# Kernel optimization log

Measured on AMD Instinct MI355X. Metric: run time of the kernel, lower is better.

The kernel has to match this reference:

```python
import jax, jax.numpy as jnp
import numpy as np

# Dimensions
B, T, H = 4, 4096, 2048          # batch, seq, hidden
NH = 16                           # total hash heads = (max_ngram-1)*n_head_per_ngram
PER_HEAD_VOCAB = 100000
DH = 64                           # per-head embedding dim
E = NH * DH                       # engram_hidden_size = 1024
G = 4                             # hc_mult
K = 4                             # kernel_size
DIL = 3                           # dilation = max_ngram_size
EPS_RMS = 1.1920929e-07           # torch RMSNorm default eps (fp32 finfo eps)
EPS_SC = 1e-5                     # ShortConv RMSNorm eps


def setup_inputs() -> dict:
    key = jax.random.key(0)
    ks = jax.random.split(key, 12)
    hidden_states = jax.random.normal(ks[0], (T, B, H), dtype=jnp.float32)
    hash_ids = jax.random.randint(ks[1], (B, T, NH), 0, PER_HEAD_VOCAB)
    emb_table = jax.random.normal(ks[2], (NH * PER_HEAD_VOCAB, DH), dtype=jnp.float32)
    s = 0.02
    key_W = jax.random.normal(ks[3], (G, H, E), dtype=jnp.float32) * s
    key_b = jax.random.normal(ks[4], (G, H), dtype=jnp.float32) * s
    value_W = jax.random.normal(ks[5], (H, E), dtype=jnp.float32) * s
    value_b = jax.random.normal(ks[6], (H,), dtype=jnp.float32) * s
    norm1_w = jnp.ones((G, H), dtype=jnp.float32)
    norm2_w = jnp.ones((G, H), dtype=jnp.float32)
    sc_norm_w = jnp.ones((G, H), dtype=jnp.float32)
    conv_w = jax.random.normal(ks[7], (G * H, K), dtype=jnp.float32) * 0.1
    return {"hidden_states": hidden_states, "hash_ids": hash_ids, "emb_table": emb_table,
            "key_W": key_W, "key_b": key_b, "value_W": value_W, "value_b": value_b,
            "norm1_w": norm1_w, "norm2_w": norm2_w, "sc_norm_w": sc_norm_w, "conv_w": conv_w}


def _rms(x, eps):
    return x * jax.lax.rsqrt(jnp.mean(x * x, axis=-1, keepdims=True) + eps)


def reference(hidden_states, hash_ids, emb_table, key_W, key_b, value_W, value_b,
              norm1_w, norm2_w, sc_norm_w, conv_w):
    # --- precompute_embeddings: hashed multi-head gather ---
    offsets = jnp.arange(NH, dtype=hash_ids.dtype) * PER_HEAD_VOCAB
    emb = emb_table[hash_ids + offsets]              # [B,T,NH,DH]
    emb = emb.reshape(B, T, E)                       # [B,T,E]

    # --- forward ---
    hs = jnp.transpose(hidden_states, (1, 0, 2))     # [B,T,H]
    # per-group key projection + RMSNorm (vectorized over G)
    keys = jnp.einsum('bte,ghe->btgh', emb, key_W) + key_b   # [B,T,G,H]
    nk = _rms(keys, EPS_RMS) * norm1_w               # [B,T,G,H]
    nq = _rms(hs, EPS_RMS)[:, :, None, :] * norm2_w  # [B,T,G,H]
    gate = jnp.sum(nk * nq, axis=-1) / np.sqrt(H)    # [B,T,G]
    gate = jnp.sqrt(jnp.maximum(jnp.abs(gate), 1e-6)) * jnp.sign(gate)
    gate = jax.nn.sigmoid(gate)[..., None]           # [B,T,G,1]
    value = gate * (emb @ value_W.T + value_b)[:, :, None, :]   # [B,T,G,H]

    # --- ShortConv: per-group RMSNorm -> causal dilated depthwise conv -> SiLU ---
    xn = _rms(value, EPS_SC) * sc_norm_w             # [B,T,G,H]
    x_bct = xn.reshape(B, T, G * H).transpose(0, 2, 1)  # [B,G*H,T]
    y = jax.lax.conv_general_dilated(
        x_bct, conv_w[:, None, :],                   # rhs [C,1,K]
        window_strides=(1,), padding=[((K - 1) * DIL, 0)],
        rhs_dilation=(DIL,), dimension_numbers=('NCH', 'OIH', 'NCH'),
        feature_group_count=G * H)                   # [B,G*H,T]
    y = jax.nn.silu(y)
    y = y.transpose(0, 2, 1).reshape(B, T, G, H)

    out = (value + y).mean(axis=2)                   # [B,T,H]
    return jnp.transpose(out, (1, 0, 2))             # [S,B,H]
```

## Files before the change

### kernel.cpp

```cpp
#include <hip/hip_runtime.h>
#include <hip/hip_bf16.h>

#define BB 4
#define TT 4096
#define HH 2048
#define NHH 16
#define VOC 100000
#define EE 1024
#define GG 4
#define BT (BB*TT)
#define NKEY (GG*HH)
#define NTOT (NKEY+HH)
#define NPART 32
#define TCV 48

static constexpr float EPS_RMS = 1.1920929e-07f;
static constexpr float EPS_SC  = 1e-5f;
static constexpr float INV_SQRT_H = 0.02209708691207961f;

using f32x4 = __attribute__((ext_vector_type(4))) float;
using s8v   = __attribute__((ext_vector_type(8))) short;
using gvoid = __attribute__((address_space(1))) const void;
using lvoid = __attribute__((address_space(3))) void;

__device__ __forceinline__ unsigned short f2bf(float f){
  union { __hip_bfloat16 h; unsigned short u; } cv;
  cv.h = __float2bfloat16(f);
  return cv.u;
}
__device__ __forceinline__ float bf2f(unsigned short u){
  union { float f; unsigned u; } cv;
  cv.u = ((unsigned)u) << 16;
  return cv.f;
}

__global__ __launch_bounds__(256) void convw_kern(const float* __restrict__ kW,
    const float* __restrict__ vW, unsigned short* __restrict__ Wc){
  const long idx  = (long)blockIdx.x*256 + threadIdx.x;
  const long base = idx*4;
  const long KN   = (long)NKEY*EE;
  float4 v;
  if (base < KN) v = *(const float4*)(kW + base);
  else           v = *(const float4*)(vW + (base - KN));
  ushort4 o; o.x=f2bf(v.x); o.y=f2bf(v.y); o.z=f2bf(v.z); o.w=f2bf(v.w);
  *(ushort4*)(Wc + base) = o;
}

__global__ __launch_bounds__(256) void prep_kern(const int* __restrict__ hids,
    const float* __restrict__ table, unsigned short* __restrict__ emb,
    const float* __restrict__ hs, float* __restrict__ rq,
    unsigned short* __restrict__ hsbf){
  const int p = blockIdx.x, tid = threadIdx.x;
  const int e = tid*4, head = e>>6, d = e&63;
  const long row = (long)hids[p*NHH + head] + (long)head*VOC;
  const float4 v = *(const float4*)(table + row*64 + d);
  ushort4 o; o.x=f2bf(v.x); o.y=f2bf(v.y); o.z=f2bf(v.z); o.w=f2bf(v.w);
  *(ushort4*)(emb + (size_t)p*EE + e) = o;
  const int b = p>>12, t = p&4095;
  const float* hrow = hs + ((size_t)t*BB + b)*HH;
  const int e8 = tid*8;
  float4 v0 = *(const float4*)(hrow+e8);
  float4 v1 = *(const float4*)(hrow+e8+4);
  ushort4 hb0; hb0.x=f2bf(v0.x); hb0.y=f2bf(v0.y); hb0.z=f2bf(v0.z); hb0.w=f2bf(v0.w);
  ushort4 hb1; hb1.x=f2bf(v1.x); hb1.y=f2bf(v1.y); hb1.z=f2bf(v1.z); hb1.w=f2bf(v1.w);
  *(ushort4*)(hsbf + (size_t)p*HH + e8)     = hb0;
  *(ushort4*)(hsbf + (size_t)p*HH + e8 + 4) = hb1;
  float s = v0.x*v0.x+v0.y*v0.y+v0.z*v0.z+v0.w*v0.w
          + v1.x*v1.x+v1.y*v1.y+v1.z*v1.z+v1.w*v1.w;
  #pragma unroll
  for (int of=32;of>=1;of>>=1) s += __shfl_xor(s,of);
  __shared__ float red[4];
  if ((tid&63)==0) red[tid>>6] = s;
  __syncthreads();
  if (tid==0){
    float tot = red[0]+red[1]+red[2]+red[3];
    rq[p] = rsqrtf(tot*(1.0f/HH) + EPS_RMS);
  }
}

__global__ __launch_bounds__(512, 2) void gemm8(
    const unsigned short* __restrict__ A, const unsigned short* __restrict__ Bw,
    const float* __restrict__ key_b, const float* __restrict__ value_b,
    const float* __restrict__ n1w, const float* __restrict__ n2w,
    const unsigned short* __restrict__ hsbf, unsigned short* __restrict__ vlinb,
    float* __restrict__ sumsqp, float* __restrict__ dotp, float* __restrict__ vsqp)
{
  __shared__ unsigned short sh[65536];
  const int tid = threadIdx.x, w = tid>>6, l = tid&63;
  const int wm = w>>2, wn = w&3;
  const int lg = l&15, lr = l>>4;
  const int tN = blockIdx.x, tM = blockIdx.y;
  const int Mrow0 = tM*256, Nrow0 = tN*256;

  const int lp = l>>3, lcs = (l&7)^lp;
  const size_t aoffT = (size_t)(Mrow0 + w*16 + lp)*EE + lcs*8;
  const size_t boffT = (size_t)(Nrow0 + w*16 + lp)*EE + lcs*8;
  const int c0 = lr ^ (lg&7);
  const unsigned aBase = (unsigned)(wm*8192 + lg*64);
  const unsigned bBase = (unsigned)(16384 + (wn>>1)*8192 + (wn&1)*4096 + lg*64);

  f32x4 acc[8][4] = {};
  s8v aR[2][4], bR[2][4];

#define STAGEH(ISB, H, KT, SB) { \
    const unsigned short* s0_ = ((ISB) ? (Bw + boffT) : (A + aoffT)) + (H)*131072 + (KT)*64; \
    const unsigned d0_ = (SB)*32768 + (ISB)*16384 + (H)*8192 + w*1024; \
    __builtin_amdgcn_global_load_lds((gvoid*)s0_,        (lvoid*)(sh + d0_),       16, 0, 0); \
    __builtin_amdgcn_global_load_lds((gvoid*)(s0_+8192), (lvoid*)(sh + d0_ + 512), 16, 0, 0); \
  }

#define BAR() { asm volatile("" ::: "memory"); __builtin_amdgcn_s_barrier(); asm volatile("" ::: "memory"); }

#define RD_A(CB, KK, MH) { \
    const unsigned short* p_ = sh + (CB)*32768 + aBase; \
    const unsigned ck_ = (unsigned)((c0 ^ ((KK)<<2))<<3); \
    aR[KK][0] = *(const s8v*)(p_ + ((MH)*4+0)*1024 + ck_); \
    aR[KK][1] = *(const s8v*)(p_ + ((MH)*4+1)*1024 + ck_); \
    aR[KK][2] = *(const s8v*)(p_ + ((MH)*4+2)*1024 + ck_); \
    aR[KK][3] = *(const s8v*)(p_ + ((MH)*4+3)*1024 + ck_); }

#define RD_B(CB, KK) { \
    const unsigned short* p_ = sh + (CB)*32768 + bBase; \
    const unsigned ck_ = (unsigned)((c0 ^ ((KK)<<2))<<3); \
    bR[KK][0] = *(const s8v*)(p_ + 0*1024 + ck_); \
    bR[KK][1] = *(const s8v*)(p_ + 1*1024 + ck_); \
    bR[KK][2] = *(const s8v*)(p_ + 2*1024 + ck_); \
    bR[KK][3] = *(const s8v*)(p_ + 3*1024 + ck_); }

#define MM(MH, KK) { \
    __builtin_amdgcn_s_setprio(1); \
    _Pragma("unroll") \
    for (int mf=0; mf<4; mf++) \
      _Pragma("unroll") \
      for (int nf=0; nf<4; nf++) \
        acc[(MH)*4+mf][nf] = __builtin_amdgcn_mfma_f32_16x16x32_bf16(aR[KK][mf], bR[KK][nf], acc[(MH)*4+mf][nf], 0,0,0); \
    __builtin_amdgcn_s_setprio(0); }

#define PH0(CB, SB, STKT, DOST) { \
    asm volatile("s_waitcnt vmcnt(0)" ::: "memory"); \
    BAR(); \
    if (DOST) { STAGEH(0, 0, STKT, SB); STAGEH(0, 1, STKT, SB); } \
    RD_A(CB, 0, 0); RD_B(CB, 0); \
    asm volatile("s_waitcnt lgkmcnt(0)" ::: "memory"); \
    __builtin_amdgcn_sched_barrier(0); \
    MM(0, 0); \
    BAR(); }

#define PH1(CB, SB, STKT, DOST) { \
    RD_A(CB, 1, 0); RD_B(CB, 1); \
    if (DOST) { STAGEH(1, 0, STKT, SB); STAGEH(1, 1, STKT, SB); } \
    BAR(); \
    asm volatile("s_waitcnt lgkmcnt(0)" ::: "memory"); \
    __builtin_amdgcn_sched_barrier(0); \
    MM(0, 1); \
    BAR(); }

#define PH2(CB) { \
    RD_A(CB, 0, 1); \
    BAR(); \
    asm volatile("s_waitcnt lgkmcnt(0)" ::: "memory"); \
    __builtin_amdgcn_sched_barrier(0); \
    MM(1, 0); \
    BAR(); }

#define PH3(CB) { \
    RD_A(CB, 1, 1); \
    BAR(); \
    asm volatile("s_waitcnt lgkmcnt(0)" ::: "memory"); \
    __builtin_amdgcn_sched_barrier(0); \
    MM(1, 1); \
    BAR(); }

  STAGEH(0,0,0,0); STAGEH(0,1,0,0); STAGEH(1,0,0,0); STAGEH(1,1,0,0);

  #pragma unroll 1
  for (int i=0; i<8; i++){
    const int kt = 2*i;
    PH0(0, 1, kt+1, true);
    PH1(0, 1, kt+1, true);
    PH2(0);
    PH3(0);
    PH0(1, 0, kt+2, (kt+2)<16);
    PH1(1, 0, kt+2, (kt+2)<16);
    PH2(1);
    PH3(1);
  }

#undef STAGEH
#undef BAR
#undef RD_A
#undef RD_B
#undef MM
#undef PH0
#undef PH1
#undef PH2
#undef PH3

  const bool isK = (Nrow0 < NKEY);
  float bias[4], cw[4];
  #pragma unroll
  for (int nf=0; nf<4; nf++){
    const int n = Nrow0 + wn*64 + nf*16 + lg;
    if (isK){ bias[nf] = key_b[n]; cw[nf] = n1w[n]*n2w[n]; }
    else    { bias[nf] = value_b[n-NKEY]; cw[nf] = 0.f; }
  }

  if (isK){
    unsigned short* hsT = sh;
    const int colbase = Nrow0 & (HH-1);
    #pragma unroll
    for (int pass=0; pass<16; pass++){
      const int r = pass*16 + (tid>>5);
      const int c8 = (tid&31)*8;
      const int p = Mrow0 + r;
      s8v wv = *(const s8v*)(hsbf + (size_t)p*HH + colbase + c8);
      *(s8v*)(hsT + r*256 + (c8 ^ (((r>>2)&3)<<4))) = wv;
    }
    __syncthreads();
    const int g = Nrow0 >> 11;
    const int slot = (tN&7)*4 + wn;
    #pragma unroll
    for (int mfa=0; mfa<8; mfa++){
      #pragma unroll
      for (int rr=0; rr<4; rr++){
        const int rowl = wm*128 + mfa*16 + lr*4 + rr;
        const int p = Mrow0 + rowl;
        float ssq=0.f, dt=0.f;
        #pragma unroll
        for (int nf=0; nf<4; nf++){
          const float c = acc[mfa][nf][rr] + bias[nf];
          const float hv = bf2f(hsT[rowl*256 + wn*64 + (((nf^lr))<<4) + lg]);
          ssq += c*c;
          dt  += c * cw[nf] * hv;
        }
        #pragma unroll
        for (int o=1;o<16;o<<=1){ ssq += __shfl_xor(ssq,o); dt += __shfl_xor(dt,o); }
        if (lg==0){
          sumsqp[(size_t)(p*GG+g)*NPART + slot] = ssq;
          dotp  [(size_t)(p*GG+g)*NPART + slot] = dt;
        }
      }
    }
  } else {
    const int slot = (tN-32)*4 + wn;
    const int h0 = Nrow0 - NKEY + wn*64;
    const int pbase = Mrow0 + wm*128;
    #pragma unroll
    for (int mfa=0; mfa<8; mfa++){
      #pragma unroll
      for (int rr=0; rr<4; rr++){
        const int p = pbase + mfa*16 + lr*4 + rr;
        float ssq=0.f;
        #pragma unroll
        for (int nf=0; nf<4; nf++){
          const float c = acc[mfa][nf][rr] + bias[nf];
          vlinb[(size_t)p*HH + h0 + nf*16 + lg] = f2bf(c);
          ssq += c*c;
        }
        #pragma unroll
        for (int o=1;o<16;o<<=1){ ssq += __shfl_xor(ssq,o); }
        if (lg==0) vsqp[(size_t)p*NPART + slot] = ssq;
      }
    }
  }
}

__global__ __launch_bounds__(256) void scal_kern(const float* __restrict__ sumsqp,
    const float* __restrict__ dotp, const float* __restrict__ vsqp,
    const float* __restrict__ rq, float* __restrict__ gate, float* __restrict__ av){
  const int i = blockIdx.x*256 + threadIdx.x;
  const int p = i>>2;
  float ss=0.f, dd=0.f, vv=0.f;
  #pragma unroll
  for (int j=0;j<NPART;j++){ ss += sumsqp[(size_t)i*NPART+j]; dd += dotp[(size_t)i*NPART+j]; }
  #pragma unroll
  for (int j=0;j<NPART;j++){ vv += vsqp[(size_t)p*NPART+j]; }
  const float rk = rsqrtf(ss*(1.0f/HH) + EPS_RMS);
  const float gv = rk * rq[p] * dd * INV_SQRT_H;
  const float sgn = (gv>0.f)?1.f:((gv<0.f)?-1.f:0.f);
  const float g1 = sqrtf(fmaxf(fabsf(gv),1e-6f))*sgn;
  const float gt = 1.f/(1.f+__expf(-g1));
  const float msvl = vv*(1.0f/HH);
  const float a = gt * rsqrtf(gt*gt*msvl + EPS_SC);
  gate[i]=gt; av[i]=a;
}

__device__ __forceinline__ ushort4 ldrow(const unsigned short* __restrict__ v, int b, int t, int h0){
  if (t < 0){ ushort4 z; z.x=0;z.y=0;z.z=0;z.w=0; return z; }
  return *(const ushort4*)(v + (size_t)((b<<12)|t)*HH + h0);
}
__device__ __forceinline__ void ldav(const float* __restrict__ av, int b, int t, float* a){
  if (t < 0){ a[0]=0.f;a[1]=0.f;a[2]=0.f;a[3]=0.f; }
  else { const float4 x = *(const float4*)(av + (size_t)((b<<12)|t)*GG);
         a[0]=x.x;a[1]=x.y;a[2]=x.z;a[3]=x.w; }
}

__global__ __launch_bounds__(256) void conv2_kern(const unsigned short* __restrict__ vlinb,
    const float* __restrict__ gate, const float* __restrict__ av,
    const float* __restrict__ conv_w, const float* __restrict__ scw,
    float* __restrict__ out){
  const int bx = blockIdx.x;
  const int b  = blockIdx.y;
  const int t0 = (bx>>1)*TCV;
  const int h0 = (bx&1)*1024 + threadIdx.x*4;

  float cwv[4][4][4];
  float sc4[4][4];
  #pragma unroll
  for (int g=0; g<4; g++){
    #pragma unroll
    for (int j2=0; j2<4; j2++){
      const int c = g*HH + h0 + j2;
      const float4 wv = *(const float4*)(conv_w + (size_t)c*4);
      cwv[g][j2][0]=wv.x; cwv[g][j2][1]=wv.y; cwv[g][j2][2]=wv.z; cwv[g][j2][3]=wv.w;
      sc4[g][j2] = scw[c];
    }
  }

  #pragma unroll 1
  for (int r=0; r<3; r++){
    const int tf = t0 + r;
    ushort4 w0 = ldrow(vlinb, b, tf-9, h0);
    ushort4 w1 = ldrow(vlinb, b, tf-6, h0);
    ushort4 w2 = ldrow(vlinb, b, tf-3, h0);
    ushort4 w3; w3.x=0;w3.y=0;w3.z=0;w3.w=0;
    #pragma unroll
    for (int j=0; j<16; j++){
      const int t = tf + 3*j;
      if (t < TT){
        const int p = (b<<12)|t;
        w3 = *(const ushort4*)(vlinb + (size_t)p*HH + h0);
        float a0[4],a1[4],a2[4],a3[4];
        ldav(av, b, t-9, a0); ldav(av, b, t-6, a1); ldav(av, b, t-3, a2); ldav(av, b, t, a3);
        float gt4[4];
        { const float4 x = *(const float4*)(gate + (size_t)p*GG);
          gt4[0]=x.x; gt4[1]=x.y; gt4[2]=x.z; gt4[3]=x.w; }
        float v0[4],v1[4],v2[4],v3[4];
        v0[0]=bf2f(w0.x); v0[1]=bf2f(w0.y); v0[2]=bf2f(w0.z); v0[3]=bf2f(w0.w);
        v1[0]=bf2f(w1.x); v1[1]=bf2f(w1.y); v1[2]=bf2f(w1.z); v1[3]=bf2f(w1.w);
        v2[0]=bf2f(w2.x); v2[1]=bf2f(w2.y); v2[2]=bf2f(w2.z); v2[3]=bf2f(w2.w);
        v3[0]=bf2f(w3.x); v3[1]=bf2f(w3.y); v3[2]=bf2f(w3.z); v3[3]=bf2f(w3.w);
        float4 ov;
        float res[4];
        #pragma unroll
        for (int j2=0; j2<4; j2++){
          float acc = 0.f;
          #pragma unroll
          for (int g=0; g<4; g++){
            float y = cwv[g][j2][0]*a0[g]*v0[j2]
                    + cwv[g][j2][1]*a1[g]*v1[j2]
                    + cwv[g][j2][2]*a2[g]*v2[j2]
                    + cwv[g][j2][3]*a3[g]*v3[j2];
            y *= sc4[g][j2];
            const float sy = y * (1.f/(1.f+__expf(-y)));
            acc += gt4[g]*v3[j2] + sy;
          }
          res[j2] = acc*0.25f;
        }
        ov.x=res[0]; ov.y=res[1]; ov.z=res[2]; ov.w=res[3];
        *(float4*)(out + ((size_t)t*BB + b)*HH + h0) = ov;
      }
      w0=w1; w1=w2; w2=w3;
    }
  }
}

extern "C" void kernel_launch(void* const* d_in, const int* in_sizes, int n_in,
                              void* d_out, int out_size, void* d_ws, size_t ws_size,
                              hipStream_t stream){
  (void)in_sizes; (void)n_in; (void)out_size; (void)ws_size;
  const float* hs    = (const float*)d_in[0];
  const int*   hids  = (const int*)d_in[1];
  const float* table = (const float*)d_in[2];
  const float* keyW  = (const float*)d_in[3];
  const float* keyB  = (const float*)d_in[4];
  const float* valW  = (const float*)d_in[5];
  const float* valB  = (const float*)d_in[6];
  const float* n1w   = (const float*)d_in[7];
  const float* n2w   = (const float*)d_in[8];
  const float* scw   = (const float*)d_in[9];
  const float* convw = (const float*)d_in[10];
  float* out = (float*)d_out;

  char* ws = (char*)d_ws;
  size_t off = 0;
  unsigned short* emb   = (unsigned short*)(ws+off); off += (size_t)BT*EE*2;
  unsigned short* Wc    = (unsigned short*)(ws+off); off += (size_t)NTOT*EE*2;
  unsigned short* vlinb = (unsigned short*)(ws+off); off += (size_t)BT*HH*2;
  unsigned short* hsbf  = (unsigned short*)(ws+off); off += (size_t)BT*HH*2;
  float* sumsqp = (float*)(ws+off); off += (size_t)BT*GG*NPART*4;
  float* dotp   = (float*)(ws+off); off += (size_t)BT*GG*NPART*4;
  float* vsqp   = (float*)(ws+off); off += (size_t)BT*NPART*4;
  float* rq     = (float*)(ws+off); off += (size_t)BT*4;
  float* gate   = (float*)(ws+off); off += (size_t)BT*GG*4;
  float* av     = (float*)(ws+off); off += (size_t)BT*GG*4;

  convw_kern<<<(NTOT*EE/4)/256, 256, 0, stream>>>(keyW, valW, Wc);
  prep_kern<<<BT, 256, 0, stream>>>(hids, table, emb, hs, rq, hsbf);
  dim3 gg(NTOT/256, BT/256);
  gemm8<<<gg, 512, 0, stream>>>(emb, Wc, keyB, valB, n1w, n2w, hsbf, vlinb, sumsqp, dotp, vsqp);
  scal_kern<<<(BT*GG)/256, 256, 0, stream>>>(sumsqp, dotp, vsqp, rq, gate, av);
  dim3 cg(((TT + TCV - 1)/TCV)*2, BB);
  conv2_kern<<<cg, 256, 0, stream>>>(vlinb, gate, av, convw, scw, out);
}
```

Before: 569.6 us.

## Restructure GEMM main loop with register double-buffering, XCD swizzle, and packed partials

The GEMM main loop is reorganized so LDS fragment reads for the next k-step and the next tile are issued while MFMAs run, removing most per-phase barriers and lgkmcnt waits. Workgroup IDs are remapped with an 8-way swizzle so tiles sharing A/B rows land on the same XCD for L2 reuse. The key epilogue now reads hidden-state values directly from global memory and reduces partial sums through LDS, writing sumsq and dot as a packed float2. The separate sumsq and dot buffers are merged, so the scalar kernel does one vector load per partial. This risks higher register pressure from the double-buffered fragments, plus scattered global loads in the epilogue.

```diff
diff --git a/kernel.cpp b/kernel.cpp
--- a/kernel.cpp
+++ b/kernel.cpp
@@ -19,6 +19,7 @@
 static constexpr float INV_SQRT_H = 0.02209708691207961f;
 
 using f32x4 = __attribute__((ext_vector_type(4))) float;
+using f32x2 = __attribute__((ext_vector_type(2))) float;
 using s8v   = __attribute__((ext_vector_type(8))) short;
 using gvoid = __attribute__((address_space(1))) const void;
 using lvoid = __attribute__((address_space(3))) void;
@@ -83,13 +84,15 @@
     const float* __restrict__ key_b, const float* __restrict__ value_b,
     const float* __restrict__ n1w, const float* __restrict__ n2w,
     const unsigned short* __restrict__ hsbf, unsigned short* __restrict__ vlinb,
-    float* __restrict__ sumsqp, float* __restrict__ dotp, float* __restrict__ vsqp)
+    f32x2* __restrict__ sdp, float* __restrict__ vsqp)
 {
   __shared__ unsigned short sh[65536];
   const int tid = threadIdx.x, w = tid>>6, l = tid&63;
   const int wm = w>>2, wn = w&3;
   const int lg = l&15, lr = l>>4;
-  const int tN = blockIdx.x, tM = blockIdx.y;
+  const int wg  = blockIdx.x;
+  const int swz = (wg&7)*320 + (wg>>3);
+  const int tM  = swz/40, tN = swz - tM*40;
   const int Mrow0 = tM*256, Nrow0 = tN*256;
 
   const int lp = l>>3, lcs = (l&7)^lp;
@@ -100,7 +103,7 @@
   const unsigned bBase = (unsigned)(16384 + (wn>>1)*8192 + (wn&1)*4096 + lg*64);
 
   f32x4 acc[8][4] = {};
-  s8v aR[2][4], bR[2][4];
+  s8v aR0[4], aR1[4], bR0[4], bR1[4];
 
 #define STAGEH(ISB, H, KT, SB) { \
     const unsigned short* s0_ = ((ISB) ? (Bw + boffT) : (A + aoffT)) + (H)*131072 + (KT)*64; \
@@ -108,138 +111,127 @@
     __builtin_amdgcn_global_load_lds((gvoid*)s0_,        (lvoid*)(sh + d0_),       16, 0, 0); \
     __builtin_amdgcn_global_load_lds((gvoid*)(s0_+8192), (lvoid*)(sh + d0_ + 512), 16, 0, 0); \
   }
+#define STAGE4(KT, SB) { STAGEH(0,0,KT,SB); STAGEH(0,1,KT,SB); STAGEH(1,0,KT,SB); STAGEH(1,1,KT,SB); }
 
 #define BAR() { asm volatile("" ::: "memory"); __builtin_amdgcn_s_barrier(); asm volatile("" ::: "memory"); }
 
-#define RD_A(CB, KK, MH) { \
+#define RD_A(CB, KK, MH, DST) { \
     const unsigned short* p_ = sh + (CB)*32768 + aBase; \
     const unsigned ck_ = (unsigned)((c0 ^ ((KK)<<2))<<3); \
-    aR[KK][0] = *(const s8v*)(p_ + ((MH)*4+0)*1024 + ck_); \
-    aR[KK][1] = *(const s8v*)(p_ + ((MH)*4+1)*1024 + ck_); \
-    aR[KK][2] = *(const s8v*)(p_ + ((MH)*4+2)*1024 + ck_); \
-    aR[KK][3] = *(const s8v*)(p_ + ((MH)*4+3)*1024 + ck_); }
-
-#define RD_B(CB, KK) { \
+    DST[0] = *(const s8v*)(p_ + ((MH)*4+0)*1024 + ck_); \
+    DST[1] = *(const s8v*)(p_ + ((MH)*4+1)*1024 + ck_); \
+    DST[2] = *(const s8v*)(p_ + ((MH)*4+2)*1024 + ck_); \
+    DST[3] = *(const s8v*)(p_ + ((MH)*4+3)*1024 + ck_); }
+
+#define RD_B(CB, KK, DST) { \
     const unsigned short* p_ = sh + (CB)*32768 + bBase; \
     const unsigned ck_ = (unsigned)((c0 ^ ((KK)<<2))<<3); \
-    bR[KK][0] = *(const s8v*)(p_ + 0*1024 + ck_); \
-    bR[KK][1] = *(const s8v*)(p_ + 1*1024 + ck_); \
-    bR[KK][2] = *(const s8v*)(p_ + 2*1024 + ck_); \
-    bR[KK][3] = *(const s8v*)(p_ + 3*1024 + ck_); }
-
-#define MM(MH, KK) { \
+    DST[0] = *(const s8v*)(p_ + 0*1024 + ck_); \
+    DST[1] = *(const s8v*)(p_ + 1*1024 + ck_); \
+    DST[2] = *(const s8v*)(p_ + 2*1024 + ck_); \
+    DST[3] = *(const s8v*)(p_ + 3*1024 + ck_); }
+
+#define MM(MH, AF, BF) { \
     __builtin_amdgcn_s_setprio(1); \
     _Pragma("unroll") \
     for (int mf=0; mf<4; mf++) \
       _Pragma("unroll") \
       for (int nf=0; nf<4; nf++) \
-        acc[(MH)*4+mf][nf] = __builtin_amdgcn_mfma_f32_16x16x32_bf16(aR[KK][mf], bR[KK][nf], acc[(MH)*4+mf][nf], 0,0,0); \
+        acc[(MH)*4+mf][nf] = __builtin_amdgcn_mfma_f32_16x16x32_bf16(AF[mf], BF[nf], acc[(MH)*4+mf][nf], 0,0,0); \
     __builtin_amdgcn_s_setprio(0); }
 
-#define PH0(CB, SB, STKT, DOST) { \
+#define TILE(CB, NB, KT1, DOST) { \
+    BAR(); \
+    if (DOST) STAGE4(KT1, NB); \
+    RD_A(CB,1,0,aR1); RD_B(CB,1,bR1); \
+    MM(0, aR0, bR0); \
+    RD_A(CB,0,1,aR0); \
+    MM(0, aR1, bR1); \
+    RD_A(CB,1,1,aR1); \
+    MM(1, aR0, bR0); \
     asm volatile("s_waitcnt vmcnt(0)" ::: "memory"); \
     BAR(); \
-    if (DOST) { STAGEH(0, 0, STKT, SB); STAGEH(0, 1, STKT, SB); } \
-    RD_A(CB, 0, 0); RD_B(CB, 0); \
-    asm volatile("s_waitcnt lgkmcnt(0)" ::: "memory"); \
-    __builtin_amdgcn_sched_barrier(0); \
-    MM(0, 0); \
-    BAR(); }
-
-#define PH1(CB, SB, STKT, DOST) { \
-    RD_A(CB, 1, 0); RD_B(CB, 1); \
-    if (DOST) { STAGEH(1, 0, STKT, SB); STAGEH(1, 1, STKT, SB); } \
+    RD_A(NB,0,0,aR0); RD_B(NB,0,bR0); \
+    MM(1, aR1, bR1); }
+
+#define TILE_LAST(CB) { \
     BAR(); \
-    asm volatile("s_waitcnt lgkmcnt(0)" ::: "memory"); \
-    __builtin_amdgcn_sched_barrier(0); \
-    MM(0, 1); \
-    BAR(); }
-
-#define PH2(CB) { \
-    RD_A(CB, 0, 1); \
-    BAR(); \
-    asm volatile("s_waitcnt lgkmcnt(0)" ::: "memory"); \
-    __builtin_amdgcn_sched_barrier(0); \
-    MM(1, 0); \
-    BAR(); }
-
-#define PH3(CB) { \
-    RD_A(CB, 1, 1); \
-    BAR(); \
-    asm volatile("s_waitcnt lgkmcnt(0)" ::: "memory"); \
-    __builtin_amdgcn_sched_barrier(0); \
-    MM(1, 1); \
-    BAR(); }
-
-  STAGEH(0,0,0,0); STAGEH(0,1,0,0); STAGEH(1,0,0,0); STAGEH(1,1,0,0);
+    RD_A(CB,1,0,aR1); RD_B(CB,1,bR1); \
+    MM(0, aR0, bR0); \
+    RD_A(CB,0,1,aR0); \
+    MM(0, aR1, bR1); \
+    RD_A(CB,1,1,aR1); \
+    MM(1, aR0, bR0); \
+    MM(1, aR1, bR1); }
+
+  STAGE4(0, 0);
+  asm volatile("s_waitcnt vmcnt(0)" ::: "memory");
+  BAR();
+  RD_A(0,0,0,aR0); RD_B(0,0,bR0);
 
   #pragma unroll 1
-  for (int i=0; i<8; i++){
+  for (int i=0; i<7; i++){
     const int kt = 2*i;
-    PH0(0, 1, kt+1, true);
-    PH1(0, 1, kt+1, true);
-    PH2(0);
-    PH3(0);
-    PH0(1, 0, kt+2, (kt+2)<16);
-    PH1(1, 0, kt+2, (kt+2)<16);
-    PH2(1);
-    PH3(1);
-  }
+    TILE(0, 1, kt+1, true);
+    TILE(1, 0, kt+2, true);
+  }
+  TILE(0, 1, 15, true);
+  TILE_LAST(1);
 
 #undef STAGEH
-#undef BAR
+#undef STAGE4
 #undef RD_A
 #undef RD_B
 #undef MM
-#undef PH0
-#undef PH1
-#undef PH2
-#undef PH3
+#undef TILE
+#undef TILE_LAST
+
+  BAR();
 
   const bool isK = (Nrow0 < NKEY);
-  float bias[4], cw[4];
+  float bias[4], cw[4]; int hcol[4];
   #pragma unroll
   for (int nf=0; nf<4; nf++){
     const int n = Nrow0 + wn*64 + nf*16 + lg;
+    hcol[nf] = n & (HH-1);
     if (isK){ bias[nf] = key_b[n]; cw[nf] = n1w[n]*n2w[n]; }
     else    { bias[nf] = value_b[n-NKEY]; cw[nf] = 0.f; }
   }
 
   if (isK){
-    unsigned short* hsT = sh;
-    const int colbase = Nrow0 & (HH-1);
-    #pragma unroll
-    for (int pass=0; pass<16; pass++){
-      const int r = pass*16 + (tid>>5);
-      const int c8 = (tid&31)*8;
-      const int p = Mrow0 + r;
-      s8v wv = *(const s8v*)(hsbf + (size_t)p*HH + colbase + c8);
-      *(s8v*)(hsT + r*256 + (c8 ^ (((r>>2)&3)<<4))) = wv;
-    }
-    __syncthreads();
     const int g = Nrow0 >> 11;
     const int slot = (tN&7)*4 + wn;
+    char* wreg = (char*)sh + w*16384;
     #pragma unroll
     for (int mfa=0; mfa<8; mfa++){
       #pragma unroll
       for (int rr=0; rr<4; rr++){
-        const int rowl = wm*128 + mfa*16 + lr*4 + rr;
-        const int p = Mrow0 + rowl;
+        const int rowl = mfa*16 + lr*4 + rr;
+        const int p = Mrow0 + wm*128 + rowl;
+        const unsigned short* hrow = hsbf + (size_t)p*HH;
         float ssq=0.f, dt=0.f;
         #pragma unroll
         for (int nf=0; nf<4; nf++){
           const float c = acc[mfa][nf][rr] + bias[nf];
-          const float hv = bf2f(hsT[rowl*256 + wn*64 + (((nf^lr))<<4) + lg]);
           ssq += c*c;
-          dt  += c * cw[nf] * hv;
+          dt  += c * cw[nf] * bf2f(hrow[hcol[nf]]);
         }
-        #pragma unroll
-        for (int o=1;o<16;o<<=1){ ssq += __shfl_xor(ssq,o); dt += __shfl_xor(dt,o); }
-        if (lg==0){
-          sumsqp[(size_t)(p*GG+g)*NPART + slot] = ssq;
-          dotp  [(size_t)(p*GG+g)*NPART + slot] = dt;
-        }
+        f32x2 pr; pr[0]=ssq; pr[1]=dt;
+        *(f32x2*)(wreg + rowl*128 + (((lg>>1) ^ (rowl&7))<<4) + ((lg&1)<<3)) = pr;
       }
+    }
+    #pragma unroll
+    for (int rh=0; rh<2; rh++){
+      const int r = l + rh*64;
+      float ssq=0.f, dt=0.f;
+      #pragma unroll
+      for (int c=0; c<8; c++){
+        f32x4 v = *(const f32x4*)(wreg + r*128 + ((c ^ (r&7))<<4));
+        ssq += v[0] + v[2]; dt += v[1] + v[3];
+      }
+      const int p = Mrow0 + wm*128 + r;
+      f32x2 o; o[0]=ssq; o[1]=dt;
+      sdp[(size_t)(p*GG+g)*NPART + slot] = o;
     }
   } else {
     const int slot = (tN-32)*4 + wn;
@@ -265,14 +257,15 @@
   }
 }
 
-__global__ __launch_bounds__(256) void scal_kern(const float* __restrict__ sumsqp,
-    const float* __restrict__ dotp, const float* __restrict__ vsqp,
+__global__ __launch_bounds__(256) void scal_kern(const f32x2* __restrict__ sdp,
+    const float* __restrict__ vsqp,
     const float* __restrict__ rq, float* __restrict__ gate, float* __restrict__ av){
   const int i = blockIdx.x*256 + threadIdx.x;
   const int p = i>>2;
   float ss=0.f, dd=0.f, vv=0.f;
-  #pragma unroll
-  for (int j=0;j<NPART;j++){ ss += sumsqp[(size_t)i*NPART+j]; dd += dotp[(size_t)i*NPART+j]; }
+  const f32x2* sp = sdp + (size_t)i*NPART;
+  #pragma unroll
+  for (int j=0;j<NPART;j++){ f32x2 v = sp[j]; ss += v[0]; dd += v[1]; }
   #pragma unroll
   for (int j=0;j<NPART;j++){ vv += vsqp[(size_t)p*NPART+j]; }
   const float rk = rsqrtf(ss*(1.0f/HH) + EPS_RMS);
@@ -388,8 +381,7 @@
   unsigned short* Wc    = (unsigned short*)(ws+off); off += (size_t)NTOT*EE*2;
   unsigned short* vlinb = (unsigned short*)(ws+off); off += (size_t)BT*HH*2;
   unsigned short* hsbf  = (unsigned short*)(ws+off); off += (size_t)BT*HH*2;
-  float* sumsqp = (float*)(ws+off); off += (size_t)BT*GG*NPART*4;
-  float* dotp   = (float*)(ws+off); off += (size_t)BT*GG*NPART*4;
+  f32x2* sdp    = (f32x2*)(ws+off); off += (size_t)BT*GG*NPART*8;
   float* vsqp   = (float*)(ws+off); off += (size_t)BT*NPART*4;
   float* rq     = (float*)(ws+off); off += (size_t)BT*4;
   float* gate   = (float*)(ws+off); off += (size_t)BT*GG*4;
@@ -397,9 +389,8 @@
 
   convw_kern<<<(NTOT*EE/4)/256, 256, 0, stream>>>(keyW, valW, Wc);
   prep_kern<<<BT, 256, 0, stream>>>(hids, table, emb, hs, rq, hsbf);
-  dim3 gg(NTOT/256, BT/256);
-  gemm8<<<gg, 512, 0, stream>>>(emb, Wc, keyB, valB, n1w, n2w, hsbf, vlinb, sumsqp, dotp, vsqp);
-  scal_kern<<<(BT*GG)/256, 256, 0, stream>>>(sumsqp, dotp, vsqp, rq, gate, av);
+  gemm8<<<2560, 512, 0, stream>>>(emb, Wc, keyB, valB, n1w, n2w, hsbf, vlinb, sdp, vsqp);
+  scal_kern<<<(BT*GG)/256, 256, 0, stream>>>(sdp, vsqp, rq, gate, av);
   dim3 cg(((TT + TCV - 1)/TCV)*2, BB);
   conv2_kern<<<cg, 256, 0, stream>>>(vlinb, gate, av, convw, scw, out);
 }
```

Measured after the change: 554.5 us. 2.7% less time.
